# Kernel optimization log

Measured on AMD Instinct MI355X. Metric: run time of the kernel, lower is better.

The kernel has to match this reference:

```python
import jax, jax.numpy as jnp
import numpy as np

DIM = 1024
N_HEADS = 16
HEAD_DIM = DIM // N_HEADS
MAX_SEQ_LEN = 2048
ROPE_THETA = 10000.0


def precompute_rope_freqs(head_dim, max_seq_len, theta):
    inv_freq = 1.0 / (theta ** (jnp.arange(0, head_dim, 2, dtype=jnp.float32) / head_dim))
    t = jnp.arange(max_seq_len, dtype=jnp.float32)
    freqs = jnp.outer(t, inv_freq)                      # [T, head_dim/2]
    emb = jnp.concatenate([freqs, freqs], axis=-1)      # [T, head_dim]
    return jnp.cos(emb), jnp.sin(emb)


def rotate_half(x):
    x1, x2 = jnp.split(x, 2, axis=-1)
    return jnp.concatenate([-x2, x1], axis=-1)


def apply_rope(x, cos, sin):
    # x: [B, H, T, D], cos/sin: [T, D] -> broadcast over B, H
    return x * cos[None, None] + rotate_half(x) * sin[None, None]


def setup_inputs() -> dict:
    key = jax.random.key(0)
    kx, kq, kk, kv, ko = jax.random.split(key, 5)
    s = 1.0 / np.sqrt(DIM)
    x = jax.random.normal(kx, (2, MAX_SEQ_LEN, DIM), dtype=jnp.float32)
    wq = jax.random.normal(kq, (DIM, DIM), dtype=jnp.float32) * s
    wk = jax.random.normal(kk, (DIM, DIM), dtype=jnp.float32) * s
    wv = jax.random.normal(kv, (DIM, DIM), dtype=jnp.float32) * s
    wo = jax.random.normal(ko, (DIM, DIM), dtype=jnp.float32) * s
    cos, sin = precompute_rope_freqs(HEAD_DIM, MAX_SEQ_LEN, ROPE_THETA)
    return {"x": x, "wq": wq, "wk": wk, "wv": wv, "wo": wo, "cos": cos, "sin": sin}


def reference(x, wq, wk, wv, wo, cos, sin):
    B, T, C = x.shape
    H, D = N_HEADS, HEAD_DIM
    # nn.Linear (no bias): y = x @ W.T
    q = (x @ wq.T).reshape(B, T, H, D).transpose(0, 2, 1, 3)  # [B,H,T,D]
    k = (x @ wk.T).reshape(B, T, H, D).transpose(0, 2, 1, 3)
    v = (x @ wv.T).reshape(B, T, H, D).transpose(0, 2, 1, 3)
    q = apply_rope(q, cos[:T], sin[:T])
    k = apply_rope(k, cos[:T], sin[:T])
    scale = 1.0 / jnp.sqrt(jnp.float32(D))
    scores = jnp.einsum("bhqd,bhkd->bhqk", q, k) * scale     # [B,H,T,T]
    causal = jnp.tril(jnp.ones((T, T), dtype=bool))
    scores = jnp.where(causal[None, None], scores, -jnp.inf)
    attn = jax.nn.softmax(scores, axis=-1)
    out = jnp.einsum("bhqk,bhkd->bhqd", attn, v)             # [B,H,T,D]
    out = out.transpose(0, 2, 1, 3).reshape(B, T, C)
    return out @ wo.T
```

## Files before the change

kernel.cpp:

```cpp
#include <hip/hip_runtime.h>

typedef __attribute__((ext_vector_type(8))) short short8;
typedef __attribute__((ext_vector_type(4))) float f32x4;

#define BB 2
#define TT 2048
#define HH 16
#define DD 64
#define CC 1024

__device__ __forceinline__ unsigned short f2bf(float f) {
  union { float f; unsigned int u; } v; v.f = f;
  unsigned int r = v.u + 0x7fffu + ((v.u >> 16) & 1u);
  return (unsigned short)(r >> 16);
}
__device__ __forceinline__ float bf2f(unsigned short h) {
  union { unsigned int u; float f; } v; v.u = ((unsigned int)h) << 16; return v.f;
}
__device__ __forceinline__ unsigned int cvtpk(float lo, float hi) {
  unsigned int r;
  asm("v_cvt_pk_bf16_f32 %0, %1, %2" : "=v"(r) : "v"(lo), "v"(hi));
  return r;
}

__global__ void cvt_f32_bf16(const float* __restrict__ in, unsigned short* __restrict__ out, int n) {
  int i = blockIdx.x * blockDim.x + threadIdx.x;
  int stride = gridDim.x * blockDim.x;
  for (; i < n; i += stride) out[i] = f2bf(in[i]);
}

template<bool BF16OUT>
__global__ __launch_bounds__(256) void gemm_bt(const unsigned short* __restrict__ A,
                                               const unsigned short* __restrict__ B,
                                               void* __restrict__ Cv,
                                               int M, int N, int K) {
  __shared__ unsigned short As[128 * 64];
  __shared__ unsigned short Bs[128 * 64];
  const int bm = blockIdx.y * 128, bn = blockIdx.x * 128;
  const int tid = threadIdx.x, wave = tid >> 6, lane = tid & 63;
  const int wm = (wave >> 1) * 64, wn = (wave & 1) * 64;
  const int g = lane >> 4, lr = lane & 15;
  f32x4 acc[4][4];
  #pragma unroll
  for (int i = 0; i < 4; ++i)
    #pragma unroll
    for (int j = 0; j < 4; ++j) acc[i][j] = (f32x4){0.f, 0.f, 0.f, 0.f};

  const int srow = lane >> 3, scol = (lane & 7) * 8;

  for (int k0 = 0; k0 < K; k0 += 64) {
    __syncthreads();
    #pragma unroll
    for (int c = 0; c < 4; ++c) {
      const int chunk = wave * 4 + c;
      const int row = chunk * 8 + srow;
      __builtin_amdgcn_global_load_lds(
        (const __attribute__((address_space(1))) void*)&A[(size_t)(bm + row) * K + k0 + scol],
        (__attribute__((address_space(3))) void*)&As[chunk * 512], 16, 0, 0);
      __builtin_amdgcn_global_load_lds(
        (const __attribute__((address_space(1))) void*)&B[(size_t)(bn + row) * K + k0 + scol],
        (__attribute__((address_space(3))) void*)&Bs[chunk * 512], 16, 0, 0);
    }
    __syncthreads();
    #pragma unroll
    for (int kk = 0; kk < 64; kk += 32) {
      const int kb = kk + g * 8;
      short8 af[4], bf[4];
      #pragma unroll
      for (int i = 0; i < 4; ++i) {
        af[i] = *(const short8*)&As[(wm + i * 16 + lr) * 64 + kb];
        bf[i] = *(const short8*)&Bs[(wn + i * 16 + lr) * 64 + kb];
      }
      __builtin_amdgcn_s_setprio(1);
      #pragma unroll
      for (int i = 0; i < 4; ++i)
        #pragma unroll
        for (int j = 0; j < 4; ++j)
          acc[i][j] = __builtin_amdgcn_mfma_f32_16x16x32_bf16(af[i], bf[j], acc[i][j], 0, 0, 0);
      __builtin_amdgcn_s_setprio(0);
    }
  }
  #pragma unroll
  for (int i = 0; i < 4; ++i) {
    const int row0 = bm + wm + i * 16 + g * 4;
    #pragma unroll
    for (int j = 0; j < 4; ++j) {
      const int col = bn + wn + j * 16 + lr;
      #pragma unroll
      for (int r = 0; r < 4; ++r) {
        float v = acc[i][j][r];
        if (BF16OUT) ((unsigned short*)Cv)[(size_t)(row0 + r) * N + col] = f2bf(v);
        else         ((float*)Cv)[(size_t)(row0 + r) * N + col] = v;
      }
    }
  }
}

__global__ void rope_qk(const unsigned short* __restrict__ qkv,
                        const float* __restrict__ cosb, const float* __restrict__ sinb,
                        unsigned short* __restrict__ qo, unsigned short* __restrict__ ko) {
  int idx = blockIdx.x * blockDim.x + threadIdx.x;
  int d = idx & 31;
  int h = (idx >> 5) & 15;
  int t = (idx >> 9) & 2047;
  int b = idx >> 20;
  const unsigned short* row = qkv + (size_t)(b * TT + t) * (3 * CC);
  float c = cosb[t * DD + d], s = sinb[t * DD + d];
  float q1 = bf2f(row[h * DD + d]),      q2 = bf2f(row[h * DD + d + 32]);
  float k1 = bf2f(row[CC + h * DD + d]), k2 = bf2f(row[CC + h * DD + d + 32]);
  size_t o = (((size_t)(b * HH + h)) * TT + t) * DD + d;
  const float QS = 0.125f * 1.44269504089f;
  qo[o]      = f2bf(QS * (q1 * c - q2 * s));
  qo[o + 32] = f2bf(QS * (q2 * c + q1 * s));
  ko[o]      = f2bf(k1 * c - k2 * s);
  ko[o + 32] = f2bf(k2 * c + k1 * s);
}

__global__ __launch_bounds__(256) void vtrans(const unsigned short* __restrict__ qkv,
                                              unsigned short* __restrict__ vt) {
  __shared__ unsigned short tile[64 * 72];
  const int bh = blockIdx.y, b = bh >> 4, h = bh & 15;
  const int t0 = blockIdx.x * 64;
  const int tid = threadIdx.x;
  const int r = tid >> 2, c0 = (tid & 3) * 16;
  const unsigned short* src = qkv + (size_t)(b * TT + t0 + r) * (3 * CC) + 2 * CC + h * DD + c0;
  *(short8*)&tile[r * 72 + c0]     = *(const short8*)src;
  *(short8*)&tile[r * 72 + c0 + 8] = *(const short8*)(src + 8);
  __syncthreads();
  short8 o0, o1;
  #pragma unroll
  for (int e = 0; e < 8; ++e) {
    ((unsigned short*)&o0)[e] = tile[(c0 + e) * 72 + r];
    ((unsigned short*)&o1)[e] = tile[(c0 + 8 + e) * 72 + r];
  }
  size_t dst = ((size_t)(bh * DD + r)) * TT + t0 + c0;
  *(short8*)&vt[dst]     = o0;
  *(short8*)&vt[dst + 8] = o1;
}

__global__ __launch_bounds__(256, 3) void attn6(const unsigned short* __restrict__ qb,
                                                const unsigned short* __restrict__ kb,
                                                const unsigned short* __restrict__ vt,
                                                unsigned short* __restrict__ aout) {
  __shared__ unsigned short Kbuf[2][64 * 64];
  __shared__ unsigned short Vbuf[2][64 * 64];
  __shared__ unsigned short Pw[4][16 * 72];
  const int L = blockIdx.x;
  const int xcd = L & 7, m = L >> 3;
  const int bh = xcd * 4 + (m & 3);
  const int qi = 31 - (m >> 2);
  const int qbase = qi * 64;
  const int tid = threadIdx.x, wave = tid >> 6, lane = tid & 63;
  const int g = lane >> 4, lr = lane & 15;
  const unsigned short* Qb  = qb + (size_t)bh * TT * DD;
  const unsigned short* Kb  = kb + (size_t)bh * TT * DD;
  const unsigned short* Vtb = vt + (size_t)bh * DD * TT;
  const int rowbase = qbase + wave * 16;
  const int myq = rowbase + lr;

  short8 qf[2];
  #pragma unroll
  for (int kk = 0; kk < 2; ++kk)
    qf[kk] = *(const short8*)&Qb[(size_t)myq * DD + kk * 32 + g * 8];

  f32x4 acc[4];
  #pragma unroll
  for (int j = 0; j < 4; ++j) acc[j] = (f32x4){0.f, 0.f, 0.f, 0.f};
  float m_i = -1e30f, l_i = 0.f;

  const int srow8 = lane >> 3;
  const int ssw_base = (lane & 7) * 8;

#define STAGE_KV(BUF, TI)                                                                   \
  {                                                                                         \
    const int tt = (TI);                                                                    \
    _Pragma("unroll")                                                                       \
    for (int c = 0; c < 2; ++c) {                                                           \
      const int chunk = wave * 2 + c;                                                       \
      const int row = chunk * 8 + srow8;                                                    \
      const int sw = ssw_base ^ ((row & 7) << 3);                                           \
      __builtin_amdgcn_global_load_lds(                                                     \
        (const __attribute__((address_space(1))) void*)&Kb[(size_t)(tt * 64 + row) * DD + sw], \
        (__attribute__((address_space(3))) void*)&Kbuf[BUF][chunk * 512], 16, 0, 0);        \
      __builtin_amdgcn_global_load_lds(                                                     \
        (const __attribute__((address_space(1))) void*)&Vtb[(size_t)row * TT + tt * 64 + sw], \
        (__attribute__((address_space(3))) void*)&Vbuf[BUF][chunk * 512], 16, 0, 0);        \
    }                                                                                       \
  }

  STAGE_KV(0, 0);
  __syncthreads();

  for (int t = 0; t <= qi; ++t) {
    const int cur = t & 1;
    if (t < qi) STAGE_KV(cur ^ 1, t + 1);

    f32x4 sv[4];
    #pragma unroll
    for (int j = 0; j < 4; ++j) sv[j] = (f32x4){0.f, 0.f, 0.f, 0.f};
    #pragma unroll
    for (int kk = 0; kk < 2; ++kk) {
      const int swc = (kk * 32 + g * 8) ^ ((lr & 7) << 3);
      short8 kf[4];
      #pragma unroll
      for (int j = 0; j < 4; ++j)
        kf[j] = *(const short8*)&Kbuf[cur][(j * 16 + lr) * 64 + swc];
      __builtin_amdgcn_s_setprio(1);
      #pragma unroll
      for (int j = 0; j < 4; ++j)
        sv[j] = __builtin_amdgcn_mfma_f32_16x16x32_bf16(kf[j], qf[kk], sv[j], 0, 0, 0);
      __builtin_amdgcn_s_setprio(0);
    }

    if (t == qi) {
      #pragma unroll
      for (int j = 0; j < 4; ++j)
        #pragma unroll
        for (int r = 0; r < 4; ++r)
          if (t * 64 + j * 16 + g * 4 + r > myq) sv[j][r] = -1e30f;
    }

    float mx = -1e30f;
    #pragma unroll
    for (int j = 0; j < 4; ++j)
      #pragma unroll
      for (int r = 0; r < 4; ++r) mx = fmaxf(mx, sv[j][r]);
    mx = fmaxf(mx, __shfl_xor(mx, 16, 64));
    mx = fmaxf(mx, __shfl_xor(mx, 32, 64));
    float mnew = fmaxf(m_i, mx);
    float scl = exp2f(m_i - mnew);
    m_i = mnew;
    float rs = 0.f;
    #pragma unroll
    for (int j = 0; j < 4; ++j)
      #pragma unroll
      for (int r = 0; r < 4; ++r) {
        float p = exp2f(sv[j][r] - mnew);
        sv[j][r] = p;
        rs += p;
      }
    rs += __shfl_xor(rs, 16, 64);
    rs += __shfl_xor(rs, 32, 64);
    l_i = l_i * scl + rs;
    #pragma unroll
    for (int j = 0; j < 4; ++j)
      #pragma unroll
      for (int r = 0; r < 4; ++r) acc[j][r] *= scl;

    #pragma unroll
    for (int j = 0; j < 4; ++j) {
      uint2 pk;
      pk.x = cvtpk(sv[j][0], sv[j][1]);
      pk.y = cvtpk(sv[j][2], sv[j][3]);
      *(uint2*)&Pw[wave][lr * 72 + j * 16 + g * 4] = pk;
    }
    #pragma unroll
    for (int kk = 0; kk < 2; ++kk) {
      short8 pf = *(const short8*)&Pw[wave][lr * 72 + kk * 32 + g * 8];
      const int swc = (kk * 32 + g * 8) ^ ((lr & 7) << 3);
      short8 vf[4];
      #pragma unroll
      for (int j = 0; j < 4; ++j)
        vf[j] = *(const short8*)&Vbuf[cur][(j * 16 + lr) * 64 + swc];
      __builtin_amdgcn_s_setprio(1);
      #pragma unroll
      for (int j = 0; j < 4; ++j)
        acc[j] = __builtin_amdgcn_mfma_f32_16x16x32_bf16(vf[j], pf, acc[j], 0, 0, 0);
      __builtin_amdgcn_s_setprio(0);
    }
    __syncthreads();
  }
#undef STAGE_KV

  const int b = bh >> 4, h = bh & 15;
  const float inv = 1.0f / l_i;
  size_t rowo = ((size_t)b * TT + myq) * CC + h * DD;
  #pragma unroll
  for (int j = 0; j < 4; ++j) {
    uint2 pk;
    pk.x = cvtpk(acc[j][0] * inv, acc[j][1] * inv);
    pk.y = cvtpk(acc[j][2] * inv, acc[j][3] * inv);
    *(uint2*)&aout[rowo + j * 16 + g * 4] = pk;
  }
}

extern "C" void kernel_launch(void* const* d_in, const int* in_sizes, int n_in,
                              void* d_out, int out_size, void* d_ws, size_t ws_size,
                              hipStream_t stream) {
  const float* x    = (const float*)d_in[0];
  const float* wq   = (const float*)d_in[1];
  const float* wk   = (const float*)d_in[2];
  const float* wv   = (const float*)d_in[3];
  const float* wo   = (const float*)d_in[4];
  const float* cosb = (const float*)d_in[5];
  const float* sinb = (const float*)d_in[6];
  float* out = (float*)d_out;
  char* ws = (char*)d_ws;

  const size_t MB = 1u << 20;
  unsigned short* xb    = (unsigned short*)(ws);
  unsigned short* wqkvb = (unsigned short*)(ws + 8 * MB);
  unsigned short* wob   = (unsigned short*)(ws + 14 * MB);
  unsigned short* sqkv  = (unsigned short*)(ws + 16 * MB);
  unsigned short* qb2   = (unsigned short*)(ws + 40 * MB);
  unsigned short* kb2   = (unsigned short*)(ws + 48 * MB);
  unsigned short* vtb   = (unsigned short*)(ws + 56 * MB);
  unsigned short* aoutb = (unsigned short*)(ws + 64 * MB);

  cvt_f32_bf16<<<2048, 256, 0, stream>>>(x,  xb, 4194304);
  cvt_f32_bf16<<<1024, 256, 0, stream>>>(wq, wqkvb,           1048576);
  cvt_f32_bf16<<<1024, 256, 0, stream>>>(wk, wqkvb + 1048576, 1048576);
  cvt_f32_bf16<<<1024, 256, 0, stream>>>(wv, wqkvb + 2097152, 1048576);
  cvt_f32_bf16<<<1024, 256, 0, stream>>>(wo, wob,             1048576);

  gemm_bt<true><<<dim3(24, 32), 256, 0, stream>>>(xb, wqkvb, sqkv, 4096, 3072, 1024);
  rope_qk<<<8192, 256, 0, stream>>>(sqkv, cosb, sinb, qb2, kb2);
  vtrans<<<dim3(32, 32), 256, 0, stream>>>(sqkv, vtb);
  attn6<<<1024, 256, 0, stream>>>(qb2, kb2, vtb, aoutb);
  gemm_bt<false><<<dim3(8, 32), 256, 0, stream>>>(aoutb, wob, out, 4096, 1024, 1024);
}
```

Before: 134.1 us.

## Double-buffer GEMM LDS tiles and skip softmax rescale when max grows little

```diff
diff --git a/kernel.cpp b/kernel.cpp
--- a/kernel.cpp
+++ b/kernel.cpp
@@ -34,8 +34,8 @@
                                                const unsigned short* __restrict__ B,
                                                void* __restrict__ Cv,
                                                int M, int N, int K) {
-  __shared__ unsigned short As[128 * 64];
-  __shared__ unsigned short Bs[128 * 64];
+  __shared__ unsigned short As[2][128 * 64];
+  __shared__ unsigned short Bs[2][128 * 64];
   const int bm = blockIdx.y * 128, bn = blockIdx.x * 128;
   const int tid = threadIdx.x, wave = tid >> 6, lane = tid & 63;
   const int wm = (wave >> 1) * 64, wn = (wave & 1) * 64;
@@ -48,28 +48,35 @@
 
   const int srow = lane >> 3, scol = (lane & 7) * 8;
 
-  for (int k0 = 0; k0 < K; k0 += 64) {
-    __syncthreads();
-    #pragma unroll
-    for (int c = 0; c < 4; ++c) {
-      const int chunk = wave * 4 + c;
-      const int row = chunk * 8 + srow;
-      __builtin_amdgcn_global_load_lds(
-        (const __attribute__((address_space(1))) void*)&A[(size_t)(bm + row) * K + k0 + scol],
-        (__attribute__((address_space(3))) void*)&As[chunk * 512], 16, 0, 0);
-      __builtin_amdgcn_global_load_lds(
-        (const __attribute__((address_space(1))) void*)&B[(size_t)(bn + row) * K + k0 + scol],
-        (__attribute__((address_space(3))) void*)&Bs[chunk * 512], 16, 0, 0);
-    }
-    __syncthreads();
+#define GSTAGE(DB, K0)                                                                    \
+  {                                                                                       \
+    _Pragma("unroll")                                                                     \
+    for (int c = 0; c < 4; ++c) {                                                         \
+      const int chunk = wave * 4 + c;                                                     \
+      const int row = chunk * 8 + srow;                                                   \
+      __builtin_amdgcn_global_load_lds(                                                   \
+        (const __attribute__((address_space(1))) void*)&A[(size_t)(bm + row) * K + (K0) + scol], \
+        (__attribute__((address_space(3))) void*)&As[DB][chunk * 512], 16, 0, 0);         \
+      __builtin_amdgcn_global_load_lds(                                                   \
+        (const __attribute__((address_space(1))) void*)&B[(size_t)(bn + row) * K + (K0) + scol], \
+        (__attribute__((address_space(3))) void*)&Bs[DB][chunk * 512], 16, 0, 0);         \
+    }                                                                                     \
+  }
+
+  GSTAGE(0, 0);
+  __syncthreads();
+  const int nkt = K >> 6;
+  for (int kt = 0; kt < nkt; ++kt) {
+    const int db = kt & 1;
+    if (kt + 1 < nkt) GSTAGE(db ^ 1, (kt + 1) << 6);
     #pragma unroll
     for (int kk = 0; kk < 64; kk += 32) {
       const int kb = kk + g * 8;
       short8 af[4], bf[4];
       #pragma unroll
       for (int i = 0; i < 4; ++i) {
-        af[i] = *(const short8*)&As[(wm + i * 16 + lr) * 64 + kb];
-        bf[i] = *(const short8*)&Bs[(wn + i * 16 + lr) * 64 + kb];
+        af[i] = *(const short8*)&As[db][(wm + i * 16 + lr) * 64 + kb];
+        bf[i] = *(const short8*)&Bs[db][(wn + i * 16 + lr) * 64 + kb];
       }
       __builtin_amdgcn_s_setprio(1);
       #pragma unroll
@@ -79,7 +86,10 @@
           acc[i][j] = __builtin_amdgcn_mfma_f32_16x16x32_bf16(af[i], bf[j], acc[i][j], 0, 0, 0);
       __builtin_amdgcn_s_setprio(0);
     }
-  }
+    __syncthreads();
+  }
+#undef GSTAGE
+
   #pragma unroll
   for (int i = 0; i < 4; ++i) {
     const int row0 = bm + wm + i * 16 + g * 4;
@@ -138,7 +148,7 @@
   *(short8*)&vt[dst + 8] = o1;
 }
 
-__global__ __launch_bounds__(256, 3) void attn6(const unsigned short* __restrict__ qb,
+__global__ __launch_bounds__(256, 3) void attn7(const unsigned short* __restrict__ qb,
                                                 const unsigned short* __restrict__ kb,
                                                 const unsigned short* __restrict__ vt,
                                                 unsigned short* __restrict__ aout) {
@@ -227,25 +237,28 @@
       for (int r = 0; r < 4; ++r) mx = fmaxf(mx, sv[j][r]);
     mx = fmaxf(mx, __shfl_xor(mx, 16, 64));
     mx = fmaxf(mx, __shfl_xor(mx, 32, 64));
-    float mnew = fmaxf(m_i, mx);
-    float scl = exp2f(m_i - mnew);
-    m_i = mnew;
+    if (!__all(mx - m_i <= 8.0f)) {
+      float mnew = fmaxf(m_i, mx);
+      float scl = exp2f(m_i - mnew);
+      m_i = mnew;
+      l_i *= scl;
+      #pragma unroll
+      for (int j = 0; j < 4; ++j)
+        #pragma unroll
+        for (int r = 0; r < 4; ++r) acc[j][r] *= scl;
+    }
     float rs = 0.f;
     #pragma unroll
     for (int j = 0; j < 4; ++j)
       #pragma unroll
       for (int r = 0; r < 4; ++r) {
-        float p = exp2f(sv[j][r] - mnew);
+        float p = exp2f(sv[j][r] - m_i);
         sv[j][r] = p;
         rs += p;
       }
     rs += __shfl_xor(rs, 16, 64);
     rs += __shfl_xor(rs, 32, 64);
-    l_i = l_i * scl + rs;
-    #pragma unroll
-    for (int j = 0; j < 4; ++j)
-      #pragma unroll
-      for (int r = 0; r < 4; ++r) acc[j][r] *= scl;
+    l_i += rs;
 
     #pragma unroll
     for (int j = 0; j < 4; ++j) {
@@ -316,6 +329,6 @@
   gemm_bt<true><<<dim3(24, 32), 256, 0, stream>>>(xb, wqkvb, sqkv, 4096, 3072, 1024);
   rope_qk<<<8192, 256, 0, stream>>>(sqkv, cosb, sinb, qb2, kb2);
   vtrans<<<dim3(32, 32), 256, 0, stream>>>(sqkv, vtb);
-  attn6<<<1024, 256, 0, stream>>>(qb2, kb2, vtb, aoutb);
+  attn7<<<1024, 256, 0, stream>>>(qb2, kb2, vtb, aoutb);
   gemm_bt<false><<<dim3(8, 32), 256, 0, stream>>>(aoutb, wob, out, 4096, 1024, 1024);
 }
```

After: 146.1 us. 8.9% more time.
